# Kernel optimization log

Measured on AMD Instinct MI355X. Metric: run time of the kernel, lower is better.

Reference implementation:

```python
import jax, jax.numpy as jnp
import numpy as np

N_NODES = 50000
N_EDGES = 800000
H = 128
NUM_LAYERS = 4
NUM_CLASSES = 10
NUM_GRAPHS = 256


def setup_inputs() -> dict:
    key = jax.random.key(0)
    ks = jax.random.split(key, 12)
    s = 0.05
    x = jax.random.normal(ks[0], (N_NODES, H), dtype=jnp.float32)
    edge_index = jax.random.randint(ks[1], (2, N_EDGES), 0, N_NODES, dtype=jnp.int32)
    batch = jnp.sort(jax.random.randint(ks[2], (N_NODES,), 0, NUM_GRAPHS, dtype=jnp.int32))
    W = jax.random.normal(ks[3], (NUM_LAYERS, H, H), dtype=jnp.float32) * s
    gru_w_ih = jax.random.normal(ks[4], (3 * H, H), dtype=jnp.float32) * s
    gru_w_hh = jax.random.normal(ks[5], (3 * H, H), dtype=jnp.float32) * s
    gru_b_ih = jax.random.normal(ks[6], (3 * H,), dtype=jnp.float32) * s
    gru_b_hh = jax.random.normal(ks[7], (3 * H,), dtype=jnp.float32) * s
    local_w = jax.random.normal(ks[8], (H, H), dtype=jnp.float32) * s
    local_b = jax.random.normal(ks[9], (H,), dtype=jnp.float32) * s
    global_w = jax.random.normal(ks[10], (NUM_CLASSES, H), dtype=jnp.float32) * s
    global_b = jax.random.normal(ks[11], (NUM_CLASSES,), dtype=jnp.float32) * s
    return {"x": x, "edge_index": edge_index, "batch": batch, "W": W,
            "gru_w_ih": gru_w_ih, "gru_w_hh": gru_w_hh,
            "gru_b_ih": gru_b_ih, "gru_b_hh": gru_b_hh,
            "local_w": local_w, "local_b": local_b,
            "global_w": global_w, "global_b": global_b}


def _gru_cell(a, h, w_ih, w_hh, b_ih, b_hh):
    # torch.nn.GRUCell math; gate order r, z, n
    gi = a @ w_ih.T + b_ih
    gh = h @ w_hh.T + b_hh
    i_r, i_z, i_n = jnp.split(gi, 3, axis=-1)
    h_r, h_z, h_n = jnp.split(gh, 3, axis=-1)
    r = jax.nn.sigmoid(i_r + h_r)
    z = jax.nn.sigmoid(i_z + h_z)
    n = jnp.tanh(i_n + r * h_n)
    return (1.0 - z) * n + z * h


def reference(x, edge_index, batch, W, gru_w_ih, gru_w_hh, gru_b_ih, gru_b_hh,
              local_w, local_b, global_w, global_b):
    n_nodes = x.shape[0]
    hidden = W.shape[-1]
    # GatedGraphConv pads input features up to hidden_dim
    h = x if x.shape[1] == hidden else jnp.pad(x, ((0, 0), (0, hidden - x.shape[1])))
    src, dst = edge_index[0], edge_index[1]  # messages flow src -> dst
    for l in range(W.shape[0]):
        m = h @ W[l]                                            # [N, H]
        aggr = jax.ops.segment_sum(m[src], dst, num_segments=n_nodes)  # gather+scatter-add
        h = _gru_cell(aggr, h, gru_w_ih, gru_w_hh, gru_b_ih, gru_b_hh)
    local = jax.nn.relu(h @ local_w.T + local_b)                # [N, H]
    sums = jax.ops.segment_sum(local, batch, num_segments=NUM_GRAPHS)   # [G, H]
    counts = jax.ops.segment_sum(jnp.ones((n_nodes, 1), local.dtype), batch,
                                 num_segments=NUM_GRAPHS)
    pooled = sums / jnp.maximum(counts, 1.0)                    # global_mean_pool
    out = pooled @ global_w.T + global_b                        # [G, C]
    return jax.nn.log_softmax(out, axis=-1)
```

## Files before the change

kernel.cpp:

```cpp
#include <hip/hip_runtime.h>

#define NN 50000
#define NE 800000
#define HD 128
#define NL 4
#define NC 10
#define NG 256
#define CAP 64

typedef __attribute__((ext_vector_type(8))) short short8;
typedef __attribute__((ext_vector_type(4))) float floatx4;

union frg { uint4 u; short8 s; };

__device__ __forceinline__ short8 load_frag(const ushort* p){
  frg f; f.u = *(const uint4*)p; return f.s;
}
__device__ __forceinline__ floatx4 MFMA(short8 a, short8 b, floatx4 c){
  return __builtin_amdgcn_mfma_f32_16x16x32_bf16(a, b, c, 0, 0, 0);
}

__device__ __forceinline__ ushort f2bf(float x){
  unsigned u = __float_as_uint(x);
  return (ushort)((u + 0x7FFFu + ((u >> 16) & 1u)) >> 16);
}
__device__ __forceinline__ float bf2f(ushort b){
  return __uint_as_float(((uint)b) << 16);
}
__device__ __forceinline__ float sigmf(float x){ return 1.0f/(1.0f + __expf(-x)); }
__device__ __forceinline__ float tanhff(float x){ return 2.0f/(1.0f + __expf(-2.0f*x)) - 1.0f; }

__global__ __launch_bounds__(256) void prep_weights_bf16(
    const float* __restrict__ w_hh, const float* __restrict__ local_w,
    const float* __restrict__ b_ih, const float* __restrict__ b_hh,
    ushort* __restrict__ whh_bf, ushort* __restrict__ lw_bf,
    float* __restrict__ bs)
{
  int idx = blockIdx.x*256 + threadIdx.x;
  if (idx < 49152) whh_bf[idx] = f2bf(w_hh[idx]);
  else if (idx < 65536){ int j = idx - 49152; lw_bf[j] = f2bf(local_w[j]); }
  else if (idx < 66048){
    int j = idx - 65536;
    if (j < 256)      bs[j] = b_ih[j] + b_hh[j];
    else if (j < 384) bs[j] = b_ih[j];
    else              bs[j] = b_hh[j - 128];
  }
}

__global__ __launch_bounds__(256) void veff_kernel(
    const float* __restrict__ W, const float* __restrict__ w_ih,
    ushort* __restrict__ veffT)
{
  int idx = blockIdx.x*256 + threadIdx.x;
  if (idx >= 4*49152) return;
  int l = idx / 49152, rem = idx % 49152;
  int o = rem >> 7, j = rem & 127;
  const float4* wr = (const float4*)&W[(size_t)(l*128 + j)*128];
  const float4* ir = (const float4*)&w_ih[(size_t)o*128];
  float acc = 0.f;
  #pragma unroll
  for (int q = 0; q < 32; q++){
    float4 a = wr[q], b = ir[q];
    acc += a.x*b.x + a.y*b.y + a.z*b.z + a.w*b.w;
  }
  veffT[idx] = f2bf(acc);
}

__global__ __launch_bounds__(256) void convert_x(const float4* __restrict__ x, ushort4* __restrict__ xbf)
{
  int i = blockIdx.x*256 + threadIdx.x;
  if (i < NN*HD/4){
    float4 v = x[i];
    ushort4 o; o.x=f2bf(v.x); o.y=f2bf(v.y); o.z=f2bf(v.z); o.w=f2bf(v.w);
    xbf[i] = o;
  }
}

#define NSLICE 8
#define CHUNKS 400
#define EPC (NE/CHUNKS)
__global__ __launch_bounds__(256) void fill_csr_sliced(
    const int* __restrict__ src, const int* __restrict__ dst,
    int* deg, ushort* __restrict__ csrf)
{
  int slice = blockIdx.x & (NSLICE-1);
  int chunk = blockIdx.x >> 3;
  int e0 = chunk * EPC;
  int lo = slice * (NN/NSLICE);
  int hi = lo + (NN/NSLICE);
  for (int e = e0 + threadIdx.x; e < e0 + EPC; e += 256){
    int d = dst[e];
    if (d >= lo && d < hi){
      int s = src[e];
      int pos = atomicAdd(&deg[d], 1);
      if (pos < CAP) csrf[(d << 6) + pos] = (ushort)s;
    }
  }
}

__global__ __launch_bounds__(64) void graph_ptr_kernel(const int* __restrict__ batch, int* __restrict__ gptr)
{
  int g = blockIdx.x*64 + threadIdx.x;
  if (g > NG) return;
  int lo = 0, hi = NN;
  while (lo < hi){
    int mid = (lo + hi) >> 1;
    if (batch[mid] < g) lo = mid + 1; else hi = mid;
  }
  gptr[g] = lo;
}

__global__ __launch_bounds__(256) void aggregate_bf16(
    const uint4* __restrict__ m4, const int* __restrict__ deg,
    const ushort* __restrict__ csrf, uint4* __restrict__ aggr4)
{
  int t = threadIdx.x;
  int lane16 = t & 15;
  int nid = blockIdx.x*16 + (t >> 4);
  int cnt = deg[nid]; if (cnt > CAP) cnt = CAP;
  const ushort* lst = csrf + (nid << 6);
  float a0=0.f,a1=0.f,a2=0.f,a3=0.f,a4=0.f,a5=0.f,a6=0.f,a7=0.f;
  int j = 0;
  for (; j + 3 < cnt; j += 4){
    int i0 = lst[j], i1 = lst[j+1], i2 = lst[j+2], i3 = lst[j+3];
    uint4 v0 = m4[(size_t)i0*16 + lane16];
    uint4 v1 = m4[(size_t)i1*16 + lane16];
    uint4 v2 = m4[(size_t)i2*16 + lane16];
    uint4 v3 = m4[(size_t)i3*16 + lane16];
    a0 += __uint_as_float(v0.x << 16) + __uint_as_float(v1.x << 16)
        + __uint_as_float(v2.x << 16) + __uint_as_float(v3.x << 16);
    a1 += __uint_as_float(v0.x & 0xFFFF0000u) + __uint_as_float(v1.x & 0xFFFF0000u)
        + __uint_as_float(v2.x & 0xFFFF0000u) + __uint_as_float(v3.x & 0xFFFF0000u);
    a2 += __uint_as_float(v0.y << 16) + __uint_as_float(v1.y << 16)
        + __uint_as_float(v2.y << 16) + __uint_as_float(v3.y << 16);
    a3 += __uint_as_float(v0.y & 0xFFFF0000u) + __uint_as_float(v1.y & 0xFFFF0000u)
        + __uint_as_float(v2.y & 0xFFFF0000u) + __uint_as_float(v3.y & 0xFFFF0000u);
    a4 += __uint_as_float(v0.z << 16) + __uint_as_float(v1.z << 16)
        + __uint_as_float(v2.z << 16) + __uint_as_float(v3.z << 16);
    a5 += __uint_as_float(v0.z & 0xFFFF0000u) + __uint_as_float(v1.z & 0xFFFF0000u)
        + __uint_as_float(v2.z & 0xFFFF0000u) + __uint_as_float(v3.z & 0xFFFF0000u);
    a6 += __uint_as_float(v0.w << 16) + __uint_as_float(v1.w << 16)
        + __uint_as_float(v2.w << 16) + __uint_as_float(v3.w << 16);
    a7 += __uint_as_float(v0.w & 0xFFFF0000u) + __uint_as_float(v1.w & 0xFFFF0000u)
        + __uint_as_float(v2.w & 0xFFFF0000u) + __uint_as_float(v3.w & 0xFFFF0000u);
  }
  for (; j < cnt; j++){
    int s = lst[j];
    uint4 v = m4[(size_t)s*16 + lane16];
    a0 += __uint_as_float(v.x << 16);
    a1 += __uint_as_float(v.x & 0xFFFF0000u);
    a2 += __uint_as_float(v.y << 16);
    a3 += __uint_as_float(v.y & 0xFFFF0000u);
    a4 += __uint_as_float(v.z << 16);
    a5 += __uint_as_float(v.z & 0xFFFF0000u);
    a6 += __uint_as_float(v.w << 16);
    a7 += __uint_as_float(v.w & 0xFFFF0000u);
  }
  uint4 o;
  o.x = (uint)f2bf(a0) | ((uint)f2bf(a1) << 16);
  o.y = (uint)f2bf(a2) | ((uint)f2bf(a3) << 16);
  o.z = (uint)f2bf(a4) | ((uint)f2bf(a5) << 16);
  o.w = (uint)f2bf(a6) | ((uint)f2bf(a7) << 16);
  aggr4[(size_t)nid*16 + lane16] = o;
}

__global__ __launch_bounds__(256, 3) void gru_mfma4(
    const ushort* __restrict__ sumh_bf, ushort* __restrict__ h_bf_out,
    const ushort* __restrict__ h_bf_in,
    const ushort* __restrict__ veffT, const ushort* __restrict__ whh_bf,
    const float* __restrict__ bs)
{
  __shared__ __align__(16) ushort lds_in[16384];
  __shared__ __align__(16) ushort lds_out[64*136];
  int t = threadIdx.x;
  int wv = t >> 6, lane = t & 63;
  int mrow = lane & 15, quad = lane >> 4;
  int nb = blockIdx.x * 64;

  #pragma unroll
  for (int q = 0; q < 8; q++){
    int c = wv*8 + q;
    int arr = c >> 4, tt = (c >> 2) & 3, kc = c & 3;
    const ushort* srcb = arr ? h_bf_in : sumh_bf;
    int node = nb + tt*16 + mrow; if (node >= NN) node = NN-1;
    uint4 v = *(const uint4*)&srcb[(size_t)node*HD + kc*32 + quad*8];
    *(uint4*)&lds_in[c*512 + lane*8] = v;
  }
  __syncthreads();

  #pragma unroll
  for (int ftl = 0; ftl < 2; ftl++){
    floatx4 aR[4] = {}, aZ[4] = {}, aIN[4] = {}, aHN[4] = {};
    size_t wbase = (size_t)((wv*2 + ftl)*16 + mrow)*HD + quad*8;

    short8 wih[3], whb[3];
    {
      size_t wo = wbase;
      wih[0] = load_frag(&veffT[wo]);
      wih[1] = load_frag(&veffT[128*HD + wo]);
      wih[2] = load_frag(&veffT[256*HD + wo]);
    }

    #pragma unroll
    for (int kc = 0; kc < 4; kc++){
      short8 fa[4], fh[4];
      #pragma unroll
      for (int tt = 0; tt < 4; tt++){
        fa[tt] = load_frag(&lds_in[((tt<<2) | kc)*512 + lane*8]);
        fh[tt] = load_frag(&lds_in[(16 | (tt<<2) | kc)*512 + lane*8]);
      }
      size_t wo = wbase + kc*32;
      whb[0] = load_frag(&whh_bf[wo]);
      whb[1] = load_frag(&whh_bf[128*HD + wo]);
      whb[2] = load_frag(&whh_bf[256*HD + wo]);
      #pragma unroll
      for (int tt = 0; tt < 4; tt++){
        aR[tt]  = MFMA(fa[tt], wih[0], aR[tt]);
        aZ[tt]  = MFMA(fa[tt], wih[1], aZ[tt]);
        aIN[tt] = MFMA(fa[tt], wih[2], aIN[tt]);
      }
      if (kc < 3){
        size_t wo2 = wbase + (kc+1)*32;
        wih[0] = load_frag(&veffT[wo2]);
        wih[1] = load_frag(&veffT[128*HD + wo2]);
        wih[2] = load_frag(&veffT[256*HD + wo2]);
      }
      #pragma unroll
      for (int tt = 0; tt < 4; tt++){
        aR[tt]  = MFMA(fh[tt], whb[0], aR[tt]);
        aZ[tt]  = MFMA(fh[tt], whb[1], aZ[tt]);
        aHN[tt] = MFMA(fh[tt], whb[2], aHN[tt]);
      }
    }

    int feat = wv*32 + ftl*16 + mrow;
    float br  = bs[feat], bz = bs[128+feat], bin = bs[256+feat], bhn = bs[384+feat];
    int kw = ftl*16 + mrow;
    int qq = kw >> 3, jj = kw & 7;
    #pragma unroll
    for (int tt = 0; tt < 4; tt++){
      int cho = (16 | (tt<<2) | wv)*512;
      #pragma unroll
      for (int r = 0; r < 4; r++){
        int nrow = quad*4 + r;
        float rr = sigmf(aR[tt][r] + br);
        float zz = sigmf(aZ[tt][r] + bz);
        float nn = tanhff(aIN[tt][r] + bin + rr*(aHN[tt][r] + bhn));
        float ho = bf2f(lds_in[cho + (qq*16 + nrow)*8 + jj]);
        float hv = (1.f - zz)*nn + zz*ho;
        lds_out[(tt*16 + nrow)*136 + feat] = f2bf(hv);
      }
    }
  }
  __syncthreads();

  #pragma unroll
  for (int p = 0; p < 4; p++){
    int chunk = p*256 + t;
    int node = chunk >> 4, f = (chunk & 15)*8;
    int ng = nb + node;
    if (ng < NN){
      uint4 v = *(const uint4*)&lds_out[node*136 + f];
      *(uint4*)&h_bf_out[(size_t)ng*HD + f] = v;
    }
  }
}

__global__ __launch_bounds__(256) void local_gemm_mfma(
    const ushort* __restrict__ hbf, const ushort* __restrict__ lw_bf,
    const float* __restrict__ bias, float* __restrict__ local)
{
  int wv = threadIdx.x >> 6, lane = threadIdx.x & 63;
  int mt = blockIdx.x*4 + wv;
  if (mt >= NN/16) return;
  int m0 = mt*16, mrow = lane & 15, quad = lane >> 4;
  floatx4 acc[8] = {};
  for (int kc = 0; kc < 4; kc++){
    int k0 = kc*32 + quad*8;
    short8 a = load_frag(&hbf[(size_t)(m0 + mrow)*HD + k0]);
    #pragma unroll
    for (int ft = 0; ft < 8; ft++){
      short8 b = load_frag(&lw_bf[(size_t)(ft*16 + mrow)*HD + k0]);
      acc[ft] = MFMA(a, b, acc[ft]);
    }
  }
  #pragma unroll
  for (int ft = 0; ft < 8; ft++){
    float bv = bias[ft*16 + mrow];
    #pragma unroll
    for (int r = 0; r < 4; r++){
      int n = m0 + quad*4 + r;
      local[(size_t)n*HD + ft*16 + mrow] = fmaxf(acc[ft][r] + bv, 0.f);
    }
  }
}

__global__ __launch_bounds__(256) void pool_kernel(
    const float* __restrict__ local, const int* __restrict__ gptr,
    float* __restrict__ pooled)
{
  __shared__ float4 red[8][32];
  int g = blockIdx.x;
  int lane = threadIdx.x & 31;
  int st = threadIdx.x >> 5;
  int s0 = gptr[g], s1 = gptr[g+1];
  float4 acc = make_float4(0,0,0,0);
  for (int n = s0 + st; n < s1; n += 8){
    float4 v = *(const float4*)&local[(size_t)n*HD + lane*4];
    acc.x += v.x; acc.y += v.y; acc.z += v.z; acc.w += v.w;
  }
  red[st][lane] = acc;
  __syncthreads();
  if (st == 0){
    float4 s = red[0][lane];
    #pragma unroll
    for (int i=1;i<8;i++){
      float4 v = red[i][lane];
      s.x += v.x; s.y += v.y; s.z += v.z; s.w += v.w;
    }
    float cnt = (float)(s1 - s0);
    if (cnt < 1.0f) cnt = 1.0f;
    float inv = 1.0f / cnt;
    s.x *= inv; s.y *= inv; s.z *= inv; s.w *= inv;
    *(float4*)&pooled[g*HD + lane*4] = s;
  }
}

__global__ __launch_bounds__(64) void classifier_kernel(
    const float* __restrict__ pooled,
    const float* __restrict__ gw, const float* __restrict__ gb,
    float* __restrict__ out)
{
  int g = blockIdx.x;
  int lane = threadIdx.x;
  float p0 = pooled[g*HD + lane];
  float p1 = pooled[g*HD + 64 + lane];
  float vals[NC];
  #pragma unroll
  for (int c=0;c<NC;c++){
    float s = p0*gw[c*HD + lane] + p1*gw[c*HD + 64 + lane];
    #pragma unroll
    for (int off=32; off>0; off>>=1) s += __shfl_down(s, off, 64);
    vals[c] = s;
  }
  if (lane == 0){
    float mx = -1e30f;
    #pragma unroll
    for (int c=0;c<NC;c++){ vals[c] += gb[c]; mx = fmaxf(mx, vals[c]); }
    float se = 0.f;
    #pragma unroll
    for (int c=0;c<NC;c++) se += __expf(vals[c] - mx);
    float lse = mx + __logf(se);
    #pragma unroll
    for (int c=0;c<NC;c++) out[g*NC + c] = vals[c] - lse;
  }
}

extern "C" void kernel_launch(void* const* d_in, const int* in_sizes, int n_in,
                              void* d_out, int out_size, void* d_ws, size_t ws_size,
                              hipStream_t stream)
{
  const float* x        = (const float*)d_in[0];
  const int*   ei       = (const int*)  d_in[1];
  const int*   batch    = (const int*)  d_in[2];
  const float* W        = (const float*)d_in[3];
  const float* w_ih     = (const float*)d_in[4];
  const float* w_hh     = (const float*)d_in[5];
  const float* b_ih     = (const float*)d_in[6];
  const float* b_hh     = (const float*)d_in[7];
  const float* local_w  = (const float*)d_in[8];
  const float* local_b  = (const float*)d_in[9];
  const float* global_w = (const float*)d_in[10];
  const float* global_b = (const float*)d_in[11];
  float* out = (float*)d_out;

  char* base = (char*)d_ws;
  ushort* csr_fixed = (ushort*)base;
  char*   R       = base + 25600000;
  ushort* sumh_bf = (ushort*)R;
  ushort* veffT   = (ushort*)(R + 12800000);
  ushort* whh_bf  = (ushort*)(R + 13193216);
  float*  bsums   = (float*)(R + 13291520);
  float*  local   = (float*)R;
  ushort* xbf     = (ushort*)(base + 51200000);
  ushort* hbf     = (ushort*)(base + 64000000);
  ushort* lw_bf   = (ushort*)(base + 76800000);
  float*  pooled  = (float*)(base + 76832768);
  int* deg        = (int*)(base + 76963840);
  int* gptr       = deg + NN;

  const int* esrc = ei;
  const int* edst = ei + NE;

  hipMemsetAsync(deg, 0, NN*sizeof(int), stream);
  prep_weights_bf16<<<259, 256, 0, stream>>>(w_hh, local_w, b_ih, b_hh, whh_bf, lw_bf, bsums);
  veff_kernel<<<768, 256, 0, stream>>>(W, w_ih, veffT);
  convert_x<<<6250, 256, 0, stream>>>((const float4*)x, (ushort4*)xbf);
  fill_csr_sliced<<<NSLICE*CHUNKS, 256, 0, stream>>>(esrc, edst, deg, csr_fixed);
  graph_ptr_kernel<<<5, 64, 0, stream>>>(batch, gptr);

  const ushort* hin_b = xbf;
  for (int l = 0; l < NL; l++){
    aggregate_bf16<<<3125, 256, 0, stream>>>((const uint4*)hin_b, deg, csr_fixed, (uint4*)sumh_bf);
    gru_mfma4<<<782, 256, 0, stream>>>(sumh_bf, hbf, hin_b,
                                       veffT + (size_t)l*49152, whh_bf, bsums);
    hin_b = hbf;
  }

  local_gemm_mfma<<<782, 256, 0, stream>>>(hbf, lw_bf, local_b, local);
  pool_kernel<<<NG, 256, 0, stream>>>(local, gptr, pooled);
  classifier_kernel<<<NG, 64, 0, stream>>>(pooled, global_w, global_b, out);
}
```

Baseline: 446.1 us.

## Fuse local GEMM with mean-pool via LDS staging and atomic partial sums

Merges the local linear+ReLU GEMM with global mean pooling. Each block stages its 64 rows of relu output in shared memory, reduces them per graph segment, and atomically adds the partial sums into a zeroed pooled buffer. The division by node count moves into the classifier. This removes the write and re-read of a 25.6 MB fp32 intermediate and one kernel launch, at the cost of an extra memset, atomics, and a floating-point summation order that now varies between runs.

```diff
diff --git a/kernel.cpp b/kernel.cpp
--- a/kernel.cpp
+++ b/kernel.cpp
@@ -266,75 +266,70 @@
   }
 }
 
-__global__ __launch_bounds__(256) void local_gemm_mfma(
+__global__ __launch_bounds__(256) void local_pool_fused(
     const ushort* __restrict__ hbf, const ushort* __restrict__ lw_bf,
-    const float* __restrict__ bias, float* __restrict__ local)
-{
-  int wv = threadIdx.x >> 6, lane = threadIdx.x & 63;
+    const float* __restrict__ bias, const int* __restrict__ batch,
+    const int* __restrict__ gptr, float* __restrict__ pooled)
+{
+  __shared__ float lds_loc[64*130];
+  int t = threadIdx.x;
+  int wv = t >> 6, lane = t & 63;
+  int mrow = lane & 15, quad = lane >> 4;
   int mt = blockIdx.x*4 + wv;
-  if (mt >= NN/16) return;
-  int m0 = mt*16, mrow = lane & 15, quad = lane >> 4;
-  floatx4 acc[8] = {};
-  for (int kc = 0; kc < 4; kc++){
-    int k0 = kc*32 + quad*8;
-    short8 a = load_frag(&hbf[(size_t)(m0 + mrow)*HD + k0]);
+
+  if (mt < NN/16){
+    int m0 = mt*16;
+    floatx4 acc[8] = {};
+    for (int kc = 0; kc < 4; kc++){
+      int k0 = kc*32 + quad*8;
+      short8 a = load_frag(&hbf[(size_t)(m0 + mrow)*HD + k0]);
+      #pragma unroll
+      for (int ft = 0; ft < 8; ft++){
+        short8 b = load_frag(&lw_bf[(size_t)(ft*16 + mrow)*HD + k0]);
+        acc[ft] = MFMA(a, b, acc[ft]);
+      }
+    }
     #pragma unroll
     for (int ft = 0; ft < 8; ft++){
-      short8 b = load_frag(&lw_bf[(size_t)(ft*16 + mrow)*HD + k0]);
-      acc[ft] = MFMA(a, b, acc[ft]);
-    }
-  }
-  #pragma unroll
-  for (int ft = 0; ft < 8; ft++){
-    float bv = bias[ft*16 + mrow];
-    #pragma unroll
-    for (int r = 0; r < 4; r++){
-      int n = m0 + quad*4 + r;
-      local[(size_t)n*HD + ft*16 + mrow] = fmaxf(acc[ft][r] + bv, 0.f);
-    }
-  }
-}
-
-__global__ __launch_bounds__(256) void pool_kernel(
-    const float* __restrict__ local, const int* __restrict__ gptr,
-    float* __restrict__ pooled)
-{
-  __shared__ float4 red[8][32];
-  int g = blockIdx.x;
-  int lane = threadIdx.x & 31;
-  int st = threadIdx.x >> 5;
-  int s0 = gptr[g], s1 = gptr[g+1];
-  float4 acc = make_float4(0,0,0,0);
-  for (int n = s0 + st; n < s1; n += 8){
-    float4 v = *(const float4*)&local[(size_t)n*HD + lane*4];
-    acc.x += v.x; acc.y += v.y; acc.z += v.z; acc.w += v.w;
-  }
-  red[st][lane] = acc;
+      float bv = bias[ft*16 + mrow];
+      #pragma unroll
+      for (int r = 0; r < 4; r++){
+        lds_loc[(wv*16 + quad*4 + r)*130 + ft*16 + mrow] = fmaxf(acc[ft][r] + bv, 0.f);
+      }
+    }
+  } else {
+    #pragma unroll
+    for (int rr = 0; rr < 16; rr++){
+      int row = wv*16 + rr;
+      for (int f = lane; f < 128; f += 64) lds_loc[row*130 + f] = 0.f;
+    }
+  }
   __syncthreads();
-  if (st == 0){
-    float4 s = red[0][lane];
-    #pragma unroll
-    for (int i=1;i<8;i++){
-      float4 v = red[i][lane];
-      s.x += v.x; s.y += v.y; s.z += v.z; s.w += v.w;
-    }
-    float cnt = (float)(s1 - s0);
-    if (cnt < 1.0f) cnt = 1.0f;
-    float inv = 1.0f / cnt;
-    s.x *= inv; s.y *= inv; s.z *= inv; s.w *= inv;
-    *(float4*)&pooled[g*HD + lane*4] = s;
+
+  int nb = blockIdx.x*64;
+  int nend = min(nb + 64, NN);
+  int feat = t & 127, slot = t >> 7;
+  int g0 = batch[nb];
+  int g1 = batch[nend - 1];
+  for (int g = g0 + slot; g <= g1; g += 2){
+    int lo = max(gptr[g], nb), hi = min(gptr[g+1], nend);
+    float s = 0.f;
+    for (int n = lo; n < hi; n++) s += lds_loc[(n - nb)*130 + feat];
+    if (hi > lo) atomicAdd(&pooled[g*HD + feat], s);
   }
 }
 
 __global__ __launch_bounds__(64) void classifier_kernel(
-    const float* __restrict__ pooled,
+    const float* __restrict__ pooled, const int* __restrict__ gptr,
     const float* __restrict__ gw, const float* __restrict__ gb,
     float* __restrict__ out)
 {
   int g = blockIdx.x;
   int lane = threadIdx.x;
-  float p0 = pooled[g*HD + lane];
-  float p1 = pooled[g*HD + 64 + lane];
+  int cnt = gptr[g+1] - gptr[g];
+  float inv = 1.0f / (float)(cnt > 0 ? cnt : 1);
+  float p0 = pooled[g*HD + lane] * inv;
+  float p1 = pooled[g*HD + 64 + lane] * inv;
   float vals[NC];
   #pragma unroll
   for (int c=0;c<NC;c++){
@@ -381,7 +376,6 @@
   ushort* veffT   = (ushort*)(R + 12800000);
   ushort* whh_bf  = (ushort*)(R + 13193216);
   float*  bsums   = (float*)(R + 13291520);
-  float*  local   = (float*)R;
   ushort* xbf     = (ushort*)(base + 51200000);
   ushort* hbf     = (ushort*)(base + 64000000);
   ushort* lw_bf   = (ushort*)(base + 76800000);
@@ -393,6 +387,7 @@
   const int* edst = ei + NE;
 
   hipMemsetAsync(deg, 0, NN*sizeof(int), stream);
+  hipMemsetAsync(pooled, 0, NG*HD*sizeof(float), stream);
   prep_weights_bf16<<<259, 256, 0, stream>>>(w_hh, local_w, b_ih, b_hh, whh_bf, lw_bf, bsums);
   veff_kernel<<<768, 256, 0, stream>>>(W, w_ih, veffT);
   convert_x<<<6250, 256, 0, stream>>>((const float4*)x, (ushort4*)xbf);
@@ -407,7 +402,6 @@
     hin_b = hbf;
   }
 
-  local_gemm_mfma<<<782, 256, 0, stream>>>(hbf, lw_bf, local_b, local);
-  pool_kernel<<<NG, 256, 0, stream>>>(local, gptr, pooled);
-  classifier_kernel<<<NG, 64, 0, stream>>>(pooled, global_w, global_b, out);
-}
+  local_pool_fused<<<782, 256, 0, stream>>>(hbf, lw_bf, local_b, batch, gptr, pooled);
+  classifier_kernel<<<NG, 64, 0, stream>>>(pooled, gptr, global_w, global_b, out);
+}
```

New measurement: 435.0 us. -2.5%, faster.
